# Optimization experiments

Hardware: AMD Instinct MI355X
Metric: run time of the kernel (lower is better)

## Reference

```python
import jax, jax.numpy as jnp
import numpy as np

NUM_HEADS = 16
MASK_VALUE = -10000.0


def setup_inputs() -> dict:
    key = jax.random.key(0)
    ks = jax.random.split(key, 5)
    B, S, D = 2, 2048, 1024
    std = 0.02
    return {
        "hidden_states": jax.random.normal(ks[0], (B, S, D), dtype=jnp.float32),
        "wq": jax.random.normal(ks[1], (D, D), dtype=jnp.float32) * std,
        "bq": jnp.zeros((D,), dtype=jnp.float32),
        "wk": jax.random.normal(ks[2], (D, D), dtype=jnp.float32) * std,
        "bk": jnp.zeros((D,), dtype=jnp.float32),
        "wv": jax.random.normal(ks[3], (D, D), dtype=jnp.float32) * std,
        "bv": jnp.zeros((D,), dtype=jnp.float32),
        "wc": jax.random.normal(ks[4], (D, D), dtype=jnp.float32) * std,
        "bc": jnp.zeros((D,), dtype=jnp.float32),
    }


def reference(hidden_states, wq, bq, wk, bk, wv, bv, wc, bc):
    B, S, D = hidden_states.shape
    H = NUM_HEADS
    hd = D // H

    def split_heads(x):  # [B,S,D] -> [B,H,S,hd]
        return x.reshape(B, S, H, hd).transpose(0, 2, 1, 3)

    q = split_heads(hidden_states @ wq + bq)
    k = split_heads(hidden_states @ wk + bk)
    v = split_heads(hidden_states @ wv + bv)

    # eager QK^T with scale_attn_weights (divide by sqrt(head_dim))
    attn_weights = jnp.einsum("bhqd,bhkd->bhqk", q, k) / jnp.sqrt(
        jnp.asarray(hd, dtype=q.dtype))

    # causal mask (attention_mask is None, not cross-attention)
    causal = jnp.tril(jnp.ones((S, S), dtype=bool))[None, None]
    attn_weights = jnp.where(causal, attn_weights,
                             jnp.asarray(MASK_VALUE, dtype=attn_weights.dtype))

    attn_weights = jax.nn.softmax(attn_weights, axis=-1)
    # attn_dropout p=0.0 (eval) -> identity; no head_mask

    attn_output = jnp.einsum("bhqk,bhkd->bhqd", attn_weights, v)
    attn_output = attn_output.transpose(0, 2, 1, 3).reshape(B, S, D)
    attn_output = attn_output @ wc + bc  # c_proj; resid_dropout p=0 -> identity
    return attn_output, attn_weights, k, v
```

## Files before the change

### kernel.cpp

```cpp
#include <hip/hip_runtime.h>


typedef __attribute__((ext_vector_type(8))) short bf8_t;
typedef __attribute__((ext_vector_type(4))) float f4_t;

#define MFMA(a, b, c) __builtin_amdgcn_mfma_f32_16x16x32_bf16(a, b, c, 0, 0, 0)

static __device__ __forceinline__ unsigned short f2bf(float f) {
    union { float f; unsigned u; } x; x.f = f;
    unsigned u = x.u;
    return (unsigned short)((u + 0x7fffu + ((u >> 16) & 1u)) >> 16);
}

#define NE 4194304ULL
#define AW 134217728ULL


__global__ void cast_hidden(const float* __restrict__ src, unsigned short* __restrict__ dst) {
    int i = (blockIdx.x * 256 + threadIdx.x) * 4;
    float4 h = *(const float4*)(src + i);
    ushort4 o;
    o.x = f2bf(h.x); o.y = f2bf(h.y); o.z = f2bf(h.z); o.w = f2bf(h.w);
    *(ushort4*)(dst + i) = o;
}

__global__ void transpose_w(const float* __restrict__ wq, const float* __restrict__ wk,
                            const float* __restrict__ wv, const float* __restrict__ wc,
                            unsigned short* __restrict__ wqkvT, unsigned short* __restrict__ wcT) {
    __shared__ float tile[32][33];
    int z = blockIdx.z;
    const float* W = z == 0 ? wq : z == 1 ? wk : z == 2 ? wv : wc;
    unsigned short* dst = (z < 3) ? (wqkvT + (size_t)z * 1024 * 1024) : wcT;
    int x0 = blockIdx.x * 32, y0 = blockIdx.y * 32;
    int tx = threadIdx.x, ty = threadIdx.y;
#pragma unroll
    for (int i = 0; i < 4; ++i)
        tile[ty + i * 8][tx] = W[(size_t)(y0 + ty + i * 8) * 1024 + x0 + tx];
    __syncthreads();
#pragma unroll
    for (int i = 0; i < 4; ++i)
        dst[(size_t)(x0 + ty + i * 8) * 1024 + y0 + tx] = f2bf(tile[tx][ty + i * 8]);
}

__global__ __launch_bounds__(256) void gemm_qkv(
    const unsigned short* __restrict__ A, const unsigned short* __restrict__ BT,
    const float* __restrict__ bq, const float* __restrict__ bk, const float* __restrict__ bv,
    unsigned short* __restrict__ q_bf, unsigned short* __restrict__ k_bf,
    unsigned short* __restrict__ vT_bf, float* __restrict__ out_k, float* __restrict__ out_v)
{
    __shared__ __align__(16) unsigned short As[128 * 40];
    __shared__ __align__(16) unsigned short Bs[128 * 40];
    const int m0 = blockIdx.y * 128, n0 = blockIdx.x * 128;
    const int tid = threadIdx.x, w = tid >> 6, lane = tid & 63, ln = lane & 15, quad = lane >> 4;
    const int wm = (w & 1) * 64, wn = (w >> 1) * 64;
    f4_t acc[4][4] = {};

    for (int kb = 0; kb < 1024; kb += 32) {
        __syncthreads();
#pragma unroll
        for (int p = 0; p < 2; ++p) {
            int c = tid + p * 256;
            int r = c >> 2, col = (c & 3) * 8;
            *(uint4*)&As[r * 40 + col] = *(const uint4*)&A[(size_t)(m0 + r) * 1024 + kb + col];
            *(uint4*)&Bs[r * 40 + col] = *(const uint4*)&BT[(size_t)(n0 + r) * 1024 + kb + col];
        }
        __syncthreads();
        bf8_t af[4], bfr[4];
#pragma unroll
        for (int i = 0; i < 4; ++i) af[i] = *(const bf8_t*)&As[(wm + i * 16 + ln) * 40 + quad * 8];
#pragma unroll
        for (int j = 0; j < 4; ++j) bfr[j] = *(const bf8_t*)&Bs[(wn + j * 16 + ln) * 40 + quad * 8];
#pragma unroll
        for (int i = 0; i < 4; ++i)
#pragma unroll
            for (int j = 0; j < 4; ++j)
                acc[i][j] = MFMA(af[i], bfr[j], acc[i][j]);
    }
#pragma unroll
    for (int j = 0; j < 4; ++j) {
        int coln = n0 + wn + j * 16 + ln;
        int which = coln >> 10, d = coln & 1023, h = d >> 6, e = d & 63;
        float bias = which == 0 ? bq[d] : (which == 1 ? bk[d] : bv[d]);
#pragma unroll
        for (int i = 0; i < 4; ++i) {
#pragma unroll
            for (int v = 0; v < 4; ++v) {
                int row = m0 + wm + i * 16 + quad * 4 + v;
                int b = row >> 11, s = row & 2047;
                float val = acc[i][j][v] + bias;
                size_t hidx = (((size_t)(b * 16 + h)) * 2048 + s) * 64 + e;
                if (which == 0) {
                    q_bf[hidx] = f2bf(val * 0.125f);
                } else if (which == 1) {
                    k_bf[hidx] = f2bf(val);
                    out_k[hidx] = val;
                } else {
                    vT_bf[((size_t)(b * 16 + h) * 64 + e) * 2048 + s] = f2bf(val);
                    out_v[hidx] = val;
                }
            }
        }
    }
}

__global__ __launch_bounds__(256) void attn_fused(
    const unsigned short* __restrict__ q_bf,
    const unsigned short* __restrict__ k_bf,
    const unsigned short* __restrict__ vT_bf,
    float* __restrict__ attn_w,
    unsigned short* __restrict__ attnpre)
{
    __shared__ __align__(16) unsigned short Qlds[64 * 72];
    __shared__ __align__(16) unsigned short Plds[4][16 * 40];
    const int bh = blockIdx.x, qt = blockIdx.y, q0 = qt * 64;
    const int tid = threadIdx.x, w = tid >> 6, lane = tid & 63, ln = lane & 15, quad = lane >> 4;
#pragma unroll
    for (int p = 0; p < 2; ++p) {
        int c = tid + p * 256;
        int r = c >> 3, e0 = (c & 7) * 8;
        *(uint4*)&Qlds[r * 72 + e0] = *(const uint4*)&q_bf[((size_t)bh * 2048 + q0 + r) * 64 + e0];
    }
    __syncthreads();
    const int r0 = w * 16;
    const int growbase = q0 + r0;
    const int rmax = growbase + 15;
    bf8_t af0 = *(const bf8_t*)&Qlds[(r0 + ln) * 72 + quad * 8];
    bf8_t af1 = *(const bf8_t*)&Qlds[(r0 + ln) * 72 + 32 + quad * 8];
    const unsigned short* kb_base = k_bf + (size_t)bh * 2048 * 64;

    f4_t lsum = {0.f, 0.f, 0.f, 0.f};
    const int nkt = (rmax >> 4) + 1;
    for (int kt = 0; kt < nkt; ++kt) {
        int col0 = kt * 16;
        const unsigned short* kp = kb_base + (size_t)(col0 + ln) * 64 + quad * 8;
        bf8_t b0 = *(const bf8_t*)kp;
        bf8_t b1 = *(const bf8_t*)(kp + 32);
        f4_t sc = {0.f, 0.f, 0.f, 0.f};
        sc = MFMA(af0, b0, sc);
        sc = MFMA(af1, b1, sc);
        int col = col0 + ln;
#pragma unroll
        for (int v = 0; v < 4; ++v) {
            int row = growbase + quad * 4 + v;
            if (col <= row) lsum[v] += __expf(sc[v]);
        }
    }
#pragma unroll
    for (int m = 1; m < 16; m <<= 1) {
#pragma unroll
        for (int v = 0; v < 4; ++v) lsum[v] += __shfl_xor(lsum[v], m);
    }
    float linv[4];
#pragma unroll
    for (int v = 0; v < 4; ++v) linv[v] = 1.f / lsum[v];

    f4_t oacc[4] = {};
    float* awp = attn_w + (size_t)bh * 2048 * 2048;
    const unsigned short* vt_base = vT_bf + (size_t)bh * 64 * 2048;
    for (int kc = 0; kc < 64; ++kc) {
        int cbase = kc * 32;
        bool needed = (cbase <= rmax);
#pragma unroll
        for (int sub = 0; sub < 2; ++sub) {
            int col0 = cbase + sub * 16;
            int col = col0 + ln;
            f4_t p = {0.f, 0.f, 0.f, 0.f};
            if (col0 <= rmax) {
                const unsigned short* kp = kb_base + (size_t)(col0 + ln) * 64 + quad * 8;
                bf8_t b0 = *(const bf8_t*)kp;
                bf8_t b1 = *(const bf8_t*)(kp + 32);
                f4_t sc = {0.f, 0.f, 0.f, 0.f};
                sc = MFMA(af0, b0, sc);
                sc = MFMA(af1, b1, sc);
#pragma unroll
                for (int v = 0; v < 4; ++v) {
                    int row = growbase + quad * 4 + v;
                    p[v] = (col <= row) ? __expf(sc[v]) * linv[v] : 0.f;
                }
            }
#pragma unroll
            for (int v = 0; v < 4; ++v) {
                awp[(size_t)(growbase + quad * 4 + v) * 2048 + col] = p[v];
                Plds[w][(quad * 4 + v) * 40 + sub * 16 + ln] = f2bf(p[v]);
            }
        }
        if (needed) {
            bf8_t pf = *(const bf8_t*)&Plds[w][ln * 40 + quad * 8];
#pragma unroll
            for (int j = 0; j < 4; ++j) {
                const unsigned short* vp = vt_base + (size_t)(j * 16 + ln) * 2048 + cbase + quad * 8;
                bf8_t vb = *(const bf8_t*)vp;
                oacc[j] = MFMA(pf, vb, oacc[j]);
            }
        }
    }
    int b = bh >> 4, h = bh & 15;
#pragma unroll
    for (int j = 0; j < 4; ++j) {
#pragma unroll
        for (int v = 0; v < 4; ++v) {
            int s = growbase + quad * 4 + v;
            int e = j * 16 + ln;
            attnpre[(size_t)(b * 2048 + s) * 1024 + h * 64 + e] = f2bf(oacc[j][v]);
        }
    }
}

__global__ __launch_bounds__(256) void gemm_cproj(
    const unsigned short* __restrict__ A,
    const unsigned short* __restrict__ BT,
    const float* __restrict__ bc, float* __restrict__ out)
{
    __shared__ __align__(16) unsigned short As[128 * 40];
    __shared__ __align__(16) unsigned short Bs[128 * 40];
    const int m0 = blockIdx.y * 128, n0 = blockIdx.x * 128;
    const int tid = threadIdx.x, w = tid >> 6, lane = tid & 63, ln = lane & 15, quad = lane >> 4;
    const int wm = (w & 1) * 64, wn = (w >> 1) * 64;
    f4_t acc[4][4] = {};

    for (int kb = 0; kb < 1024; kb += 32) {
        __syncthreads();
#pragma unroll
        for (int p = 0; p < 2; ++p) {
            int c = tid + p * 256;
            int r = c >> 2, col = (c & 3) * 8;
            *(uint4*)&As[r * 40 + col] = *(const uint4*)&A[(size_t)(m0 + r) * 1024 + kb + col];
            *(uint4*)&Bs[r * 40 + col] = *(const uint4*)&BT[(size_t)(n0 + r) * 1024 + kb + col];
        }
        __syncthreads();
        bf8_t af[4], bfr[4];
#pragma unroll
        for (int i = 0; i < 4; ++i) af[i] = *(const bf8_t*)&As[(wm + i * 16 + ln) * 40 + quad * 8];
#pragma unroll
        for (int j = 0; j < 4; ++j) bfr[j] = *(const bf8_t*)&Bs[(wn + j * 16 + ln) * 40 + quad * 8];
#pragma unroll
        for (int i = 0; i < 4; ++i)
#pragma unroll
            for (int j = 0; j < 4; ++j)
                acc[i][j] = MFMA(af[i], bfr[j], acc[i][j]);
    }
#pragma unroll
    for (int j = 0; j < 4; ++j) {
        int coln = n0 + wn + j * 16 + ln;
        float bias = bc[coln];
#pragma unroll
        for (int i = 0; i < 4; ++i) {
#pragma unroll
            for (int v = 0; v < 4; ++v) {
                int row = m0 + wm + i * 16 + quad * 4 + v;
                out[(size_t)row * 1024 + coln] = acc[i][j][v] + bias;
            }
        }
    }
}

extern "C" void kernel_launch(void* const* d_in, const int* in_sizes, int n_in,
                              void* d_out, int out_size, void* d_ws, size_t ws_size,
                              hipStream_t stream)
{
    const float* hs = (const float*)d_in[0];
    const float* wq = (const float*)d_in[1];
    const float* bq = (const float*)d_in[2];
    const float* wk = (const float*)d_in[3];
    const float* bk = (const float*)d_in[4];
    const float* wv = (const float*)d_in[5];
    const float* bv = (const float*)d_in[6];
    const float* wc = (const float*)d_in[7];
    const float* bc = (const float*)d_in[8];

    float* out      = (float*)d_out;
    float* out_aw   = out + NE;
    float* out_k    = out_aw + AW;
    float* out_v    = out_k + NE;

    char* ws = (char*)d_ws;
    unsigned short* hid_bf  = (unsigned short*)(ws);
    unsigned short* wqkvT   = (unsigned short*)(ws + 8388608);
    unsigned short* wcT     = (unsigned short*)(ws + 14680064);
    unsigned short* q_bf    = (unsigned short*)(ws + 16777216);
    unsigned short* k_bf    = (unsigned short*)(ws + 25165824);
    unsigned short* vT_bf   = (unsigned short*)(ws + 33554432);
    unsigned short* attnpre = (unsigned short*)(ws + 41943040);

    cast_hidden<<<4096, 256, 0, stream>>>(hs, hid_bf);
    transpose_w<<<dim3(32, 32, 4), dim3(32, 8), 0, stream>>>(wq, wk, wv, wc, wqkvT, wcT);
    gemm_qkv<<<dim3(24, 32), 256, 0, stream>>>(hid_bf, wqkvT, bq, bk, bv,
                                               q_bf, k_bf, vT_bf, out_k, out_v);
    attn_fused<<<dim3(32, 32), 256, 0, stream>>>(q_bf, k_bf, vT_bf, out_aw, attnpre);
    gemm_cproj<<<dim3(8, 32), 256, 0, stream>>>(attnpre, wcT, bc, out);
}
```

Measured before the change: 918.4 us.

## Use direct global-to-LDS swizzled GEMM staging and 128-row attention tiles with vectorized stores

The GEMM kernels now stage A/B tiles with global_load_lds into an XOR-swizzled LDS layout and use a K-step of 64 instead of 32, which halves the barrier count and avoids register round trips. The attention kernel now processes 128 query rows per block, two 16-row strips per wave, so each K/V fragment load is shared by both strips. The probability tile is staged through fp32 LDS so attention weights can be written as coalesced float4 rows. Blocks are launched heaviest-first for causal load balance. The costs are more LDS use and higher register pressure per block, plus fewer attention blocks in flight.

```diff
diff --git a/kernel.cpp b/kernel.cpp
--- a/kernel.cpp
+++ b/kernel.cpp
@@ -10,6 +10,12 @@
     union { float f; unsigned u; } x; x.f = f;
     unsigned u = x.u;
     return (unsigned short)((u + 0x7fffu + ((u >> 16) & 1u)) >> 16);
+}
+
+static __device__ __forceinline__ void stage16(const unsigned short* g, unsigned short* lbase) {
+    __builtin_amdgcn_global_load_lds(
+        (const __attribute__((address_space(1))) unsigned int*)g,
+        (__attribute__((address_space(3))) unsigned int*)lbase, 16, 0, 0);
 }
 
 #define NE 4194304ULL
@@ -42,40 +48,51 @@
         dst[(size_t)(x0 + ty + i * 8) * 1024 + y0 + tx] = f2bf(tile[tx][ty + i * 8]);
 }
 
+
+#define GEMM_CORE(A_, B_, KDIM)                                                             \
+    const int m0 = blockIdx.y * 128, n0 = blockIdx.x * 128;                                 \
+    const int tid = threadIdx.x, w = tid >> 6, lane = tid & 63, ln = lane & 15,             \
+              quad = lane >> 4;                                                             \
+    const int wm = (w & 1) * 64, wn = (w >> 1) * 64;                                        \
+    f4_t acc[4][4] = {};                                                                    \
+    for (int kb = 0; kb < (KDIM); kb += 64) {                                               \
+        __syncthreads();                                                                    \
+        _Pragma("unroll")                                                                   \
+        for (int p = 0; p < 4; ++p) {                                                       \
+            int t = (w * 4 + p) * 64 + lane;                                                \
+            int r = t >> 3, c = (t & 7) ^ (r & 7);                                          \
+            stage16(&(A_)[(size_t)(m0 + r) * (KDIM) + kb + c * 8], &As[(w * 4 + p) * 512]); \
+            stage16(&(B_)[(size_t)(n0 + r) * (KDIM) + kb + c * 8], &Bs[(w * 4 + p) * 512]); \
+        }                                                                                   \
+        __syncthreads();                                                                    \
+        bf8_t af[2][4], bfm[2][4];                                                          \
+        _Pragma("unroll")                                                                   \
+        for (int h = 0; h < 2; ++h) {                                                       \
+            _Pragma("unroll")                                                               \
+            for (int i = 0; i < 4; ++i) {                                                   \
+                int c = (h * 4 + quad) ^ (ln & 7);                                          \
+                af[h][i] = *(const bf8_t*)&As[(wm + i * 16 + ln) * 64 + c * 8];             \
+                bfm[h][i] = *(const bf8_t*)&Bs[(wn + i * 16 + ln) * 64 + c * 8];            \
+            }                                                                               \
+        }                                                                                   \
+        _Pragma("unroll")                                                                   \
+        for (int h = 0; h < 2; ++h)                                                         \
+            _Pragma("unroll")                                                               \
+            for (int i = 0; i < 4; ++i)                                                     \
+                _Pragma("unroll")                                                           \
+                for (int j = 0; j < 4; ++j)                                                 \
+                    acc[i][j] = MFMA(af[h][i], bfm[h][j], acc[i][j]);                       \
+    }
+
 __global__ __launch_bounds__(256) void gemm_qkv(
     const unsigned short* __restrict__ A, const unsigned short* __restrict__ BT,
     const float* __restrict__ bq, const float* __restrict__ bk, const float* __restrict__ bv,
     unsigned short* __restrict__ q_bf, unsigned short* __restrict__ k_bf,
     unsigned short* __restrict__ vT_bf, float* __restrict__ out_k, float* __restrict__ out_v)
 {
-    __shared__ __align__(16) unsigned short As[128 * 40];
-    __shared__ __align__(16) unsigned short Bs[128 * 40];
-    const int m0 = blockIdx.y * 128, n0 = blockIdx.x * 128;
-    const int tid = threadIdx.x, w = tid >> 6, lane = tid & 63, ln = lane & 15, quad = lane >> 4;
-    const int wm = (w & 1) * 64, wn = (w >> 1) * 64;
-    f4_t acc[4][4] = {};
-
-    for (int kb = 0; kb < 1024; kb += 32) {
-        __syncthreads();
-#pragma unroll
-        for (int p = 0; p < 2; ++p) {
-            int c = tid + p * 256;
-            int r = c >> 2, col = (c & 3) * 8;
-            *(uint4*)&As[r * 40 + col] = *(const uint4*)&A[(size_t)(m0 + r) * 1024 + kb + col];
-            *(uint4*)&Bs[r * 40 + col] = *(const uint4*)&BT[(size_t)(n0 + r) * 1024 + kb + col];
-        }
-        __syncthreads();
-        bf8_t af[4], bfr[4];
-#pragma unroll
-        for (int i = 0; i < 4; ++i) af[i] = *(const bf8_t*)&As[(wm + i * 16 + ln) * 40 + quad * 8];
-#pragma unroll
-        for (int j = 0; j < 4; ++j) bfr[j] = *(const bf8_t*)&Bs[(wn + j * 16 + ln) * 40 + quad * 8];
-#pragma unroll
-        for (int i = 0; i < 4; ++i)
-#pragma unroll
-            for (int j = 0; j < 4; ++j)
-                acc[i][j] = MFMA(af[i], bfr[j], acc[i][j]);
-    }
+    __shared__ __align__(16) unsigned short As[128 * 64];
+    __shared__ __align__(16) unsigned short Bs[128 * 64];
+    GEMM_CORE(A, BT, 1024)
 #pragma unroll
     for (int j = 0; j < 4; ++j) {
         int coln = n0 + wn + j * 16 + ln;
@@ -103,6 +120,28 @@
     }
 }
 
+__global__ __launch_bounds__(256) void gemm_cproj(
+    const unsigned short* __restrict__ A, const unsigned short* __restrict__ BT,
+    const float* __restrict__ bc, float* __restrict__ out)
+{
+    __shared__ __align__(16) unsigned short As[128 * 64];
+    __shared__ __align__(16) unsigned short Bs[128 * 64];
+    GEMM_CORE(A, BT, 1024)
+#pragma unroll
+    for (int j = 0; j < 4; ++j) {
+        int coln = n0 + wn + j * 16 + ln;
+        float bias = bc[coln];
+#pragma unroll
+        for (int i = 0; i < 4; ++i) {
+#pragma unroll
+            for (int v = 0; v < 4; ++v) {
+                int row = m0 + wm + i * 16 + quad * 4 + v;
+                out[(size_t)row * 1024 + coln] = acc[i][j][v] + bias;
+            }
+        }
+    }
+}
+
 __global__ __launch_bounds__(256) void attn_fused(
     const unsigned short* __restrict__ q_bf,
     const unsigned short* __restrict__ k_bf,
@@ -110,146 +149,128 @@
     float* __restrict__ attn_w,
     unsigned short* __restrict__ attnpre)
 {
-    __shared__ __align__(16) unsigned short Qlds[64 * 72];
-    __shared__ __align__(16) unsigned short Plds[4][16 * 40];
-    const int bh = blockIdx.x, qt = blockIdx.y, q0 = qt * 64;
+    __shared__ __align__(16) unsigned short Qlds[128 * 72];
+    __shared__ __align__(16) float Pf32[4][16 * 36];
+    const int bh = blockIdx.x;
+    const int q0 = (15 - blockIdx.y) * 128;
     const int tid = threadIdx.x, w = tid >> 6, lane = tid & 63, ln = lane & 15, quad = lane >> 4;
 #pragma unroll
-    for (int p = 0; p < 2; ++p) {
+    for (int p = 0; p < 4; ++p) {
         int c = tid + p * 256;
         int r = c >> 3, e0 = (c & 7) * 8;
         *(uint4*)&Qlds[r * 72 + e0] = *(const uint4*)&q_bf[((size_t)bh * 2048 + q0 + r) * 64 + e0];
     }
     __syncthreads();
-    const int r0 = w * 16;
-    const int growbase = q0 + r0;
-    const int rmax = growbase + 15;
-    bf8_t af0 = *(const bf8_t*)&Qlds[(r0 + ln) * 72 + quad * 8];
-    bf8_t af1 = *(const bf8_t*)&Qlds[(r0 + ln) * 72 + 32 + quad * 8];
+    const int s0 = w * 16, s1 = 64 + w * 16;
+    const int g0 = q0 + s0, g1 = q0 + s1;
+    const int rmax0 = g0 + 15, rmax1 = g1 + 15;
+    bf8_t aA0 = *(const bf8_t*)&Qlds[(s0 + ln) * 72 + quad * 8];
+    bf8_t aA1 = *(const bf8_t*)&Qlds[(s0 + ln) * 72 + 32 + quad * 8];
+    bf8_t aB0 = *(const bf8_t*)&Qlds[(s1 + ln) * 72 + quad * 8];
+    bf8_t aB1 = *(const bf8_t*)&Qlds[(s1 + ln) * 72 + 32 + quad * 8];
     const unsigned short* kb_base = k_bf + (size_t)bh * 2048 * 64;
 
-    f4_t lsum = {0.f, 0.f, 0.f, 0.f};
-    const int nkt = (rmax >> 4) + 1;
+    f4_t l0v = {0.f, 0.f, 0.f, 0.f}, l1v = {0.f, 0.f, 0.f, 0.f};
+    const f4_t zf = {0.f, 0.f, 0.f, 0.f};
+    const int nkt = (rmax1 >> 4) + 1;
     for (int kt = 0; kt < nkt; ++kt) {
-        int col0 = kt * 16;
+        int col0 = kt * 16, col = col0 + ln;
         const unsigned short* kp = kb_base + (size_t)(col0 + ln) * 64 + quad * 8;
         bf8_t b0 = *(const bf8_t*)kp;
         bf8_t b1 = *(const bf8_t*)(kp + 32);
-        f4_t sc = {0.f, 0.f, 0.f, 0.f};
-        sc = MFMA(af0, b0, sc);
-        sc = MFMA(af1, b1, sc);
-        int col = col0 + ln;
+        f4_t sc = MFMA(aB0, b0, zf); sc = MFMA(aB1, b1, sc);
 #pragma unroll
         for (int v = 0; v < 4; ++v) {
-            int row = growbase + quad * 4 + v;
-            if (col <= row) lsum[v] += __expf(sc[v]);
+            if (col <= g1 + quad * 4 + v) l1v[v] += __expf(sc[v]);
+        }
+        if (col0 <= rmax0) {
+            f4_t sc0 = MFMA(aA0, b0, zf); sc0 = MFMA(aA1, b1, sc0);
+#pragma unroll
+            for (int v = 0; v < 4; ++v) {
+                if (col <= g0 + quad * 4 + v) l0v[v] += __expf(sc0[v]);
+            }
         }
     }
 #pragma unroll
     for (int m = 1; m < 16; m <<= 1) {
 #pragma unroll
-        for (int v = 0; v < 4; ++v) lsum[v] += __shfl_xor(lsum[v], m);
-    }
-    float linv[4];
-#pragma unroll
-    for (int v = 0; v < 4; ++v) linv[v] = 1.f / lsum[v];
-
-    f4_t oacc[4] = {};
+        for (int v = 0; v < 4; ++v) {
+            l0v[v] += __shfl_xor(l0v[v], m);
+            l1v[v] += __shfl_xor(l1v[v], m);
+        }
+    }
+    f4_t linv0, linv1;
+#pragma unroll
+    for (int v = 0; v < 4; ++v) { linv0[v] = 1.f / l0v[v]; linv1[v] = 1.f / l1v[v]; }
+
+    f4_t o0[4] = {}, o1[4] = {};
     float* awp = attn_w + (size_t)bh * 2048 * 2048;
     const unsigned short* vt_base = vT_bf + (size_t)bh * 64 * 2048;
+    float* pw = &Pf32[w][0];
     for (int kc = 0; kc < 64; ++kc) {
-        int cbase = kc * 32;
-        bool needed = (cbase <= rmax);
-#pragma unroll
-        for (int sub = 0; sub < 2; ++sub) {
-            int col0 = cbase + sub * 16;
-            int col = col0 + ln;
-            f4_t p = {0.f, 0.f, 0.f, 0.f};
-            if (col0 <= rmax) {
-                const unsigned short* kp = kb_base + (size_t)(col0 + ln) * 64 + quad * 8;
-                bf8_t b0 = *(const bf8_t*)kp;
-                bf8_t b1 = *(const bf8_t*)(kp + 32);
-                f4_t sc = {0.f, 0.f, 0.f, 0.f};
-                sc = MFMA(af0, b0, sc);
-                sc = MFMA(af1, b1, sc);
-#pragma unroll
-                for (int v = 0; v < 4; ++v) {
-                    int row = growbase + quad * 4 + v;
-                    p[v] = (col <= row) ? __expf(sc[v]) * linv[v] : 0.f;
+        int col0c = kc * 32;
+        bool act1 = col0c <= rmax1, act0 = col0c <= rmax0;
+        bf8_t kf[4], vb[4];
+        if (act1) {
+#pragma unroll
+            for (int sub = 0; sub < 2; ++sub) {
+                const unsigned short* kp = kb_base + (size_t)(col0c + sub * 16 + ln) * 64 + quad * 8;
+                kf[sub * 2] = *(const bf8_t*)kp;
+                kf[sub * 2 + 1] = *(const bf8_t*)(kp + 32);
+            }
+#pragma unroll
+            for (int j = 0; j < 4; ++j)
+                vb[j] = *(const bf8_t*)(vt_base + (size_t)(j * 16 + ln) * 2048 + col0c + quad * 8);
+        }
+        auto do_strip = [&](int gb, bf8_t a0, bf8_t a1, const f4_t& linv, f4_t* oacc, bool active) {
+            if (active) {
+#pragma unroll
+                for (int sub = 0; sub < 2; ++sub) {
+                    f4_t sc = MFMA(a0, kf[sub * 2], zf);
+                    sc = MFMA(a1, kf[sub * 2 + 1], sc);
+                    int col = col0c + sub * 16 + ln;
+#pragma unroll
+                    for (int v = 0; v < 4; ++v) {
+                        int row = gb + quad * 4 + v;
+                        float p = (col <= row) ? __expf(sc[v]) * linv[v] : 0.f;
+                        pw[(quad * 4 + v) * 36 + sub * 16 + ln] = p;
+                    }
                 }
-            }
-#pragma unroll
-            for (int v = 0; v < 4; ++v) {
-                awp[(size_t)(growbase + quad * 4 + v) * 2048 + col] = p[v];
-                Plds[w][(quad * 4 + v) * 40 + sub * 16 + ln] = f2bf(p[v]);
-            }
-        }
-        if (needed) {
-            bf8_t pf = *(const bf8_t*)&Plds[w][ln * 40 + quad * 8];
-#pragma unroll
-            for (int j = 0; j < 4; ++j) {
-                const unsigned short* vp = vt_base + (size_t)(j * 16 + ln) * 2048 + cbase + quad * 8;
-                bf8_t vb = *(const bf8_t*)vp;
-                oacc[j] = MFMA(pf, vb, oacc[j]);
-            }
-        }
+#pragma unroll
+                for (int half = 0; half < 2; ++half) {
+                    int r = half * 8 + (lane >> 3), cq = lane & 7;
+                    float4 val = *(const float4*)&pw[r * 36 + cq * 4];
+                    *(float4*)&awp[(size_t)(gb + r) * 2048 + col0c + cq * 4] = val;
+                }
+                float4 pa = *(const float4*)&pw[ln * 36 + quad * 8];
+                float4 pb = *(const float4*)&pw[ln * 36 + quad * 8 + 4];
+                bf8_t pf;
+                pf[0] = (short)f2bf(pa.x); pf[1] = (short)f2bf(pa.y);
+                pf[2] = (short)f2bf(pa.z); pf[3] = (short)f2bf(pa.w);
+                pf[4] = (short)f2bf(pb.x); pf[5] = (short)f2bf(pb.y);
+                pf[6] = (short)f2bf(pb.z); pf[7] = (short)f2bf(pb.w);
+#pragma unroll
+                for (int j = 0; j < 4; ++j) oacc[j] = MFMA(pf, vb[j], oacc[j]);
+            } else {
+                float4 z4 = {0.f, 0.f, 0.f, 0.f};
+#pragma unroll
+                for (int half = 0; half < 2; ++half) {
+                    int r = half * 8 + (lane >> 3), cq = lane & 7;
+                    *(float4*)&awp[(size_t)(gb + r) * 2048 + col0c + cq * 4] = z4;
+                }
+            }
+        };
+        do_strip(g1, aB0, aB1, linv1, o1, act1);
+        do_strip(g0, aA0, aA1, linv0, o0, act0);
     }
     int b = bh >> 4, h = bh & 15;
 #pragma unroll
     for (int j = 0; j < 4; ++j) {
 #pragma unroll
         for (int v = 0; v < 4; ++v) {
-            int s = growbase + quad * 4 + v;
-            int e = j * 16 + ln;
-            attnpre[(size_t)(b * 2048 + s) * 1024 + h * 64 + e] = f2bf(oacc[j][v]);
-        }
-    }
-}
-
-__global__ __launch_bounds__(256) void gemm_cproj(
-    const unsigned short* __restrict__ A,
-    const unsigned short* __restrict__ BT,
-    const float* __restrict__ bc, float* __restrict__ out)
-{
-    __shared__ __align__(16) unsigned short As[128 * 40];
-    __shared__ __align__(16) unsigned short Bs[128 * 40];
-    const int m0 = blockIdx.y * 128, n0 = blockIdx.x * 128;
-    const int tid = threadIdx.x, w = tid >> 6, lane = tid & 63, ln = lane & 15, quad = lane >> 4;
-    const int wm = (w & 1) * 64, wn = (w >> 1) * 64;
-    f4_t acc[4][4] = {};
-
-    for (int kb = 0; kb < 1024; kb += 32) {
-        __syncthreads();
-#pragma unroll
-        for (int p = 0; p < 2; ++p) {
-            int c = tid + p * 256;
-            int r = c >> 2, col = (c & 3) * 8;
-            *(uint4*)&As[r * 40 + col] = *(const uint4*)&A[(size_t)(m0 + r) * 1024 + kb + col];
-            *(uint4*)&Bs[r * 40 + col] = *(const uint4*)&BT[(size_t)(n0 + r) * 1024 + kb + col];
-        }
-        __syncthreads();
-        bf8_t af[4], bfr[4];
-#pragma unroll
-        for (int i = 0; i < 4; ++i) af[i] = *(const bf8_t*)&As[(wm + i * 16 + ln) * 40 + quad * 8];
-#pragma unroll
-        for (int j = 0; j < 4; ++j) bfr[j] = *(const bf8_t*)&Bs[(wn + j * 16 + ln) * 40 + quad * 8];
-#pragma unroll
-        for (int i = 0; i < 4; ++i)
-#pragma unroll
-            for (int j = 0; j < 4; ++j)
-                acc[i][j] = MFMA(af[i], bfr[j], acc[i][j]);
-    }
-#pragma unroll
-    for (int j = 0; j < 4; ++j) {
-        int coln = n0 + wn + j * 16 + ln;
-        float bias = bc[coln];
-#pragma unroll
-        for (int i = 0; i < 4; ++i) {
-#pragma unroll
-            for (int v = 0; v < 4; ++v) {
-                int row = m0 + wm + i * 16 + quad * 4 + v;
-                out[(size_t)row * 1024 + coln] = acc[i][j][v] + bias;
-            }
+            int e = h * 64 + j * 16 + ln;
+            attnpre[(size_t)(b * 2048 + g0 + quad * 4 + v) * 1024 + e] = f2bf(o0[j][v]);
+            attnpre[(size_t)(b * 2048 + g1 + quad * 4 + v) * 1024 + e] = f2bf(o1[j][v]);
         }
     }
 }
@@ -286,6 +307,6 @@
     transpose_w<<<dim3(32, 32, 4), dim3(32, 8), 0, stream>>>(wq, wk, wv, wc, wqkvT, wcT);
     gemm_qkv<<<dim3(24, 32), 256, 0, stream>>>(hid_bf, wqkvT, bq, bk, bv,
                                                q_bf, k_bf, vT_bf, out_k, out_v);
-    attn_fused<<<dim3(32, 32), 256, 0, stream>>>(q_bf, k_bf, vT_bf, out_aw, attnpre);
+    attn_fused<<<dim3(32, 16), 256, 0, stream>>>(q_bf, k_bf, vT_bf, out_aw, attnpre);
     gemm_cproj<<<dim3(8, 32), 256, 0, stream>>>(attnpre, wcT, bc, out);
 }
```

New measurement: 810.4 us. 1.13x faster.
